# Optimization experiments

Hardware: AMD Instinct MI355X
Metric: run time of the kernel (lower is better)

The kernel has to match this reference:

```python
import jax, jax.numpy as jnp
import numpy as np

B, S, H, NH = 4, 2048, 1024, 16
HD = H // NH
EPS = 1e-12


def setup_inputs() -> dict:
    key = jax.random.key(0)
    ks = jax.random.split(key, 12)
    sc = 0.02
    return {
        "query": jax.random.normal(ks[0], (B, S, H), dtype=jnp.float32),
        "attention_mask": jnp.zeros((B, 1, 1, S), dtype=jnp.float32),
        "Wq": jax.random.normal(ks[1], (H, H), dtype=jnp.float32) * sc,
        "bq": jnp.zeros((H,), dtype=jnp.float32),
        "Wk": jax.random.normal(ks[2], (H, H), dtype=jnp.float32) * sc,
        "bk": jnp.zeros((H,), dtype=jnp.float32),
        "Wv": jax.random.normal(ks[3], (H, H), dtype=jnp.float32) * sc,
        "bv": jnp.zeros((H,), dtype=jnp.float32),
        "Wd": jax.random.normal(ks[4], (H, H), dtype=jnp.float32) * sc,
        "bd": jnp.zeros((H,), dtype=jnp.float32),
        "ln_gamma": jnp.ones((H,), dtype=jnp.float32),
        "ln_beta": jnp.zeros((H,), dtype=jnp.float32),
    }


def reference(query, attention_mask, Wq, bq, Wk, bk, Wv, bv, Wd, bd, ln_gamma, ln_beta):
    # QKV projections: [B,S,H] -> [B,S,NH,HD]
    q = (query @ Wq + bq).reshape(B, S, NH, HD)
    k = (query @ Wk + bk).reshape(B, S, NH, HD)
    v = (query @ Wv + bv).reshape(B, S, NH, HD)
    # scores: [B,NH,S,S]
    scores = jnp.einsum("bqhd,bkhd->bhqk", q, k) / jnp.sqrt(jnp.float32(HD))
    scores = scores + attention_mask
    probs = jax.nn.softmax(scores, axis=-1)  # attn_dropout p=0 (eval)
    ctx = jnp.einsum("bhqk,bkhd->bqhd", probs, v).reshape(B, S, H)
    hidden = ctx @ Wd + bd  # out_dropout p=0 (eval)
    # pre-LN residual path: LN(hidden) + query
    mu = jnp.mean(hidden, axis=-1, keepdims=True)
    var = jnp.mean(jnp.square(hidden - mu), axis=-1, keepdims=True)
    hidden = (hidden - mu) * jax.lax.rsqrt(var + EPS) * ln_gamma + ln_beta
    return hidden + query
```

## Files before the change

### kernel.cpp

```cpp
#include <hip/hip_runtime.h>
#include <stdint.h>

#define Bn 4
#define Sn 2048
#define Hn 1024
#define NHn 16
#define Mn 8192

typedef unsigned short bf_t;
typedef __attribute__((ext_vector_type(8))) short s16x8;
typedef __attribute__((ext_vector_type(4))) short s16x4;
typedef __attribute__((ext_vector_type(8))) unsigned short u16x8;
typedef __attribute__((ext_vector_type(4))) unsigned short u16x4;
typedef __attribute__((ext_vector_type(4))) float f32x4;
typedef __attribute__((ext_vector_type(4))) unsigned int u32x4;
typedef __attribute__((ext_vector_type(2))) unsigned int u32x2;

__device__ __forceinline__ bf_t f2bf(float f) {
  unsigned int u = __float_as_uint(f);
  u += 0x7fffu + ((u >> 16) & 1u);
  return (bf_t)(u >> 16);
}

__device__ __forceinline__ unsigned pk2(float lo, float hi) {
  return __builtin_amdgcn_perm(__float_as_uint(hi), __float_as_uint(lo), 0x07060302u);
}
__device__ __forceinline__ s16x4 pack4(float a0, float a1, float a2, float a3) {
  u32x2 t;
  t[0] = pk2(a0, a1);
  t[1] = pk2(a2, a3);
  return __builtin_bit_cast(s16x4, t);
}

#define MFMA16K16(a, b, c) __builtin_amdgcn_mfma_f32_16x16x16bf16_1k(a, b, c, 0, 0, 0)

#define GLOAD16(gp, lp) __builtin_amdgcn_global_load_lds(              \
    (__attribute__((address_space(1))) void*)(gp),                     \
    (__attribute__((address_space(3))) void*)(lp), 16, 0, 0)

__global__ __launch_bounds__(256)
void prep(const float* __restrict__ Wq, const float* __restrict__ Wk,
          const float* __restrict__ Wv, const float* __restrict__ Wd,
          const float* __restrict__ query,
          bf_t* __restrict__ Wt, bf_t* __restrict__ Wdt, bf_t* __restrict__ Xb) {
  __shared__ float tile[32][33];
  const int z = blockIdx.z;
  const int tx = threadIdx.x;
  const int ty = threadIdx.y;
  if (z == 4) {
    const int bid = blockIdx.y * 32 + blockIdx.x;
    const int t = ty * 32 + tx;
    const size_t base = (size_t)bid * 8192 + t * 4;
#pragma unroll
    for (int i = 0; i < 8; i++) {
      const f32x4 v = *(const f32x4*)(query + base + i * 1024);
      u16x4 o;
      o[0] = f2bf(v[0]); o[1] = f2bf(v[1]); o[2] = f2bf(v[2]); o[3] = f2bf(v[3]);
      *(u16x4*)(Xb + base + i * 1024) = o;
    }
    return;
  }
  const float* W = (z == 0) ? Wq : (z == 1) ? Wk : (z == 2) ? Wv : Wd;
  bf_t* dst = (z < 3) ? Wt + (size_t)z * Hn * Hn : Wdt;
  const int n0 = blockIdx.x * 32, k0 = blockIdx.y * 32;
#pragma unroll
  for (int i = 0; i < 4; i++)
    tile[ty + i * 8][tx] = W[(size_t)(k0 + ty + i * 8) * Hn + n0 + tx];
  __syncthreads();
#pragma unroll
  for (int i = 0; i < 4; i++) {
    const int nn = ty + i * 8, kk = tx;
    dst[(size_t)(n0 + nn) * Hn + k0 + kk] = f2bf(tile[kk][nn]);
  }
}

__global__ __launch_bounds__(256, 3)
void gemm_bt(const bf_t* __restrict__ A, const bf_t* __restrict__ Bt,
             const float* __restrict__ b0, const float* __restrict__ b1,
             const float* __restrict__ b2, void* __restrict__ outp,
             int N, int K, int out_bf16)
{
  __shared__ bf_t As[2][4096];
  __shared__ bf_t Bs[2][4096];
  const int tid = threadIdx.x;
  const int wave = tid >> 6, lane = tid & 63;
  const int l15 = lane & 15, quad = lane >> 4;
  const int bm = blockIdx.y * 128, bn = blockIdx.x * 128;
  const int wm = (wave >> 1) * 64, wn = (wave & 1) * 64;
  const int srow = tid >> 2;
  const int scol = (tid & 3) * 8;

  const bf_t* Ag = A + (size_t)(bm + srow) * K + scol;
  const bf_t* Bg = Bt + (size_t)(bn + srow) * K + scol;

  f32x4 acc[4][4] = {};

  GLOAD16(Ag, As[0] + tid * 8);
  GLOAD16(Ag + (size_t)64 * K, As[0] + 2048 + tid * 8);
  GLOAD16(Bg, Bs[0] + tid * 8);
  GLOAD16(Bg + (size_t)64 * K, Bs[0] + 2048 + tid * 8);

  const int nIter = K >> 5;
  for (int i = 0; i < nIter; i++) {
    const int cur = i & 1;
    __syncthreads();
    if (i + 1 < nIter) {
      const int k0 = (i + 1) * 32;
      GLOAD16(Ag + k0, As[cur ^ 1] + tid * 8);
      GLOAD16(Ag + (size_t)64 * K + k0, As[cur ^ 1] + 2048 + tid * 8);
      GLOAD16(Bg + k0, Bs[cur ^ 1] + tid * 8);
      GLOAD16(Bg + (size_t)64 * K + k0, Bs[cur ^ 1] + 2048 + tid * 8);
    }
    s16x8 af[4], bfr[4];
#pragma unroll
    for (int mi = 0; mi < 4; mi++)
      af[mi] = *(const s16x8*)&As[cur][(wm + mi * 16 + l15) * 32 + quad * 8];
#pragma unroll
    for (int ni = 0; ni < 4; ni++)
      bfr[ni] = *(const s16x8*)&Bs[cur][(wn + ni * 16 + l15) * 32 + quad * 8];
#pragma unroll
    for (int mi = 0; mi < 4; mi++)
#pragma unroll
      for (int ni = 0; ni < 4; ni++)
        acc[mi][ni] = __builtin_amdgcn_mfma_f32_16x16x32_bf16(af[mi], bfr[ni], acc[mi][ni], 0, 0, 0);
  }

#pragma unroll
  for (int ni = 0; ni < 4; ni++) {
    const int gn = bn + wn + ni * 16 + l15;
    const float* bp = (gn < 1024) ? b0 : ((gn < 2048) ? b1 : b2);
    const float bias = bp[gn & 1023];
#pragma unroll
    for (int mi = 0; mi < 4; mi++) {
#pragma unroll
      for (int r = 0; r < 4; r++) {
        const int gm = bm + wm + mi * 16 + quad * 4 + r;
        const float v = acc[mi][ni][r] + bias;
        if (out_bf16) ((bf_t*)outp)[(size_t)gm * N + gn] = f2bf(v);
        else          ((float*)outp)[(size_t)gm * N + gn] = v;
      }
    }
  }
}

__global__ __launch_bounds__(256)
void kvswz(const bf_t* __restrict__ qkv, bf_t* __restrict__ Kf,
           bf_t* __restrict__ Vf, const float* __restrict__ mask,
           float* __restrict__ mask2) {
  __shared__ u32x4 smbuf[640];
  const int t = threadIdx.x;
  const int bh = blockIdx.y, b = bh >> 4, h = bh & 15;
  const int k0 = blockIdx.x * 64;

  if (blockIdx.z == 0) {
    bf_t* KT = (bf_t*)smbuf;
#pragma unroll
    for (int i = 0; i < 2; i++) {
      const int c = t + i * 256;
      const int row = c >> 3, col8 = (c & 7) * 8;
      const u16x8 v = *(const u16x8*)(qkv + (size_t)(b * Sn + k0 + row) * 3072 + 1024 + h * 64 + col8);
      *(u16x8*)&KT[row * 80 + col8] = v;
    }
    __syncthreads();
    bf_t* dst0 = Kf + ((size_t)(bh * 32 + blockIdx.x) * 8) * 512;
#pragma unroll
    for (int i = 0; i < 2; i++) {
      const int p = t + i * 256;
      const int frag = p >> 6, lane = p & 63;
      const int ks = frag >> 1, half = frag & 1;
      const int l15 = lane & 15, quad = lane >> 4;
      const u16x8 v = *(const u16x8*)&KT[(ks * 16 + l15) * 80 + half * 32 + quad * 8];
      *(u16x8*)(dst0 + (size_t)frag * 512 + lane * 8) = v;
    }
  } else {
    unsigned int* P32 = (unsigned int*)smbuf;
    {
      const int kp = t >> 3;
      const int d0 = (t & 7) * 8;
      const bf_t* p0 = qkv + (size_t)(b * Sn + k0 + 2 * kp) * 3072 + 2048 + h * 64 + d0;
      const u16x8 r0 = *(const u16x8*)p0;
      const u16x8 r1 = *(const u16x8*)(p0 + 3072);
#pragma unroll
      for (int j = 0; j < 8; j++)
        P32[(d0 + j) * 33 + kp] = (unsigned)r0[j] | ((unsigned)r1[j] << 16);
    }
    if (h == 0 && t < 64)
      mask2[b * Sn + k0 + t] = mask[b * Sn + k0 + t] * 1.44269504f;
    __syncthreads();
    bf_t* dst0 = Vf + ((size_t)(bh * 32 + blockIdx.x) * 8) * 512;
#pragma unroll
    for (int i = 0; i < 2; i++) {
      const int p = t + i * 256;
      const int fp = p >> 6, lane = p & 63;
      const int dvblk = fp >> 1, kpair = fp & 1;
      const int l15 = lane & 15, quad = (lane >> 4) & 3;
      const int d = dvblk * 16 + l15;
      const int c = kpair * 16 + quad * 2;
      u32x4 w;
      w[0] = P32[d * 33 + c];
      w[1] = P32[d * 33 + c + 1];
      w[2] = P32[d * 33 + c + 8];
      w[3] = P32[d * 33 + c + 9];
      *(u32x4*)(dst0 + (size_t)fp * 512 + lane * 8) = w;
    }
  }
}

__global__ __launch_bounds__(256)
void attn(const bf_t* __restrict__ qkv, const bf_t* __restrict__ Kf,
          const bf_t* __restrict__ Vf, const float* __restrict__ mask2,
          bf_t* __restrict__ ctx)
{
  __shared__ bf_t Ks[2][4096];
  __shared__ bf_t Vs[2][4096];
  __shared__ float Ms[2048];

  const int tid = threadIdx.x;
  const int wave = tid >> 6, lane = tid & 63;
  const int l15 = lane & 15, quad = lane >> 4;
  const int idx = blockIdx.x;
  const int bh = idx & 63, b = bh >> 4, h = bh & 15;
  const int q0 = (idx >> 6) * 128;

  {
    const float* m2row = mask2 + (size_t)b * Sn;
    const f32x4 m0 = *(const f32x4*)(m2row + tid * 8);
    const f32x4 m1 = *(const f32x4*)(m2row + tid * 8 + 4);
    *(f32x4*)&Ms[tid * 8] = m0;
    *(f32x4*)&Ms[tid * 8 + 4] = m1;
  }

  s16x8 aq[2][2];
#pragma unroll
  for (int qf = 0; qf < 2; qf++) {
    const bf_t* qp = qkv + (size_t)(b * Sn + q0 + wave * 32 + qf * 16 + l15) * 3072 + h * 64;
    aq[qf][0] = *(const s16x8*)(qp + quad * 8);
    aq[qf][1] = *(const s16x8*)(qp + 32 + quad * 8);
  }

  f32x4 lacc[2] = {};
  f32x4 o[2][4] = {};
  const s16x4 ONES = {16256, 16256, 16256, 16256};

  const bf_t* kb = Kf + (size_t)bh * 32 * 4096;
  const bf_t* vb = Vf + (size_t)bh * 32 * 4096;

  const float C1 = 0.125f * 1.44269504f;

#pragma unroll
  for (int c = 0; c < 2; c++) {
    GLOAD16(kb + c * 2048 + tid * 8, Ks[0] + c * 2048 + tid * 8);
    GLOAD16(vb + c * 2048 + tid * 8, Vs[0] + c * 2048 + tid * 8);
  }

  for (int it = 0; it < 32; ++it) {
    const int cur = it & 1;
    __syncthreads();
    if (it < 31) {
      const bf_t* kn = kb + (size_t)(it + 1) * 4096;
      const bf_t* vn = vb + (size_t)(it + 1) * 4096;
#pragma unroll
      for (int c = 0; c < 2; c++) {
        GLOAD16(kn + c * 2048 + tid * 8, Ks[cur ^ 1] + c * 2048 + tid * 8);
        GLOAD16(vn + c * 2048 + tid * 8, Vs[cur ^ 1] + c * 2048 + tid * 8);
      }
    }

    s16x4 pb[2][4];
#pragma unroll
    for (int e = 0; e < 4; e++) {
      const s16x8 k0f = *(const s16x8*)&Ks[cur][(e * 2 + 0) * 512 + lane * 8];
      const s16x8 k1f = *(const s16x8*)&Ks[cur][(e * 2 + 1) * 512 + lane * 8];
      const f32x4 mk2 = *(const f32x4*)&Ms[it * 64 + e * 16 + quad * 4];
#pragma unroll
      for (int qf = 0; qf < 2; qf++) {
        f32x4 acc = {};
        acc = __builtin_amdgcn_mfma_f32_16x16x32_bf16(k0f, aq[qf][0], acc, 0, 0, 0);
        acc = __builtin_amdgcn_mfma_f32_16x16x32_bf16(k1f, aq[qf][1], acc, 0, 0, 0);
        const float p0 = __builtin_amdgcn_exp2f(fmaf(acc[0], C1, mk2[0]));
        const float p1 = __builtin_amdgcn_exp2f(fmaf(acc[1], C1, mk2[1]));
        const float p2 = __builtin_amdgcn_exp2f(fmaf(acc[2], C1, mk2[2]));
        const float p3 = __builtin_amdgcn_exp2f(fmaf(acc[3], C1, mk2[3]));
        pb[qf][e] = pack4(p0, p1, p2, p3);
        lacc[qf] = MFMA16K16(ONES, pb[qf][e], lacc[qf]);
      }
    }

#pragma unroll
    for (int kpair = 0; kpair < 2; kpair++)
#pragma unroll
      for (int dvblk = 0; dvblk < 4; dvblk++) {
        const s16x8 vv = *(const s16x8*)&Vs[cur][(dvblk * 2 + kpair) * 512 + lane * 8];
        const s16x4 vlo = {vv[0], vv[1], vv[2], vv[3]};
        const s16x4 vhi = {vv[4], vv[5], vv[6], vv[7]};
#pragma unroll
        for (int qf = 0; qf < 2; qf++) {
          o[qf][dvblk] = MFMA16K16(vlo, pb[qf][kpair * 2 + 0], o[qf][dvblk]);
          o[qf][dvblk] = MFMA16K16(vhi, pb[qf][kpair * 2 + 1], o[qf][dvblk]);
        }
      }
  }

#pragma unroll
  for (int qf = 0; qf < 2; qf++) {
    const float inv = 1.f / lacc[qf][0];
    const size_t row = (size_t)(b * Sn + q0 + wave * 32 + qf * 16 + l15);
#pragma unroll
    for (int dvblk = 0; dvblk < 4; dvblk++) {
      u16x4 ov;
#pragma unroll
      for (int r = 0; r < 4; r++) ov[r] = f2bf(o[qf][dvblk][r] * inv);
      *(u16x4*)&ctx[row * Hn + h * 64 + dvblk * 16 + quad * 4] = ov;
    }
  }
}

__global__ __launch_bounds__(256)
void ln_res(const float* __restrict__ hid, const float* __restrict__ query,
            const float* __restrict__ gamma, const float* __restrict__ beta,
            float* __restrict__ out)
{
  const int row = blockIdx.x, t = threadIdx.x;
  const f32x4 h = *(const f32x4*)(hid + (size_t)row * Hn + t * 4);
  float s = h[0] + h[1] + h[2] + h[3];
  float ss = h[0]*h[0] + h[1]*h[1] + h[2]*h[2] + h[3]*h[3];
#pragma unroll
  for (int m = 32; m; m >>= 1) { s += __shfl_xor(s, m); ss += __shfl_xor(ss, m); }
  __shared__ float red[8];
  if ((t & 63) == 0) { red[t >> 6] = s; red[4 + (t >> 6)] = ss; }
  __syncthreads();
  s = red[0] + red[1] + red[2] + red[3];
  ss = red[4] + red[5] + red[6] + red[7];
  const float mu = s * (1.f / Hn);
  const float rs = rsqrtf(ss * (1.f / Hn) - mu * mu + 1e-12f);
  const f32x4 q = *(const f32x4*)(query + (size_t)row * Hn + t * 4);
  const f32x4 g = *(const f32x4*)(gamma + t * 4);
  const f32x4 be = *(const f32x4*)(beta + t * 4);
  f32x4 o;
#pragma unroll
  for (int j = 0; j < 4; j++) o[j] = (h[j] - mu) * rs * g[j] + be[j] + q[j];
  *(f32x4*)(out + (size_t)row * Hn + t * 4) = o;
}

extern "C" void kernel_launch(void* const* d_in, const int* in_sizes, int n_in,
                              void* d_out, int out_size, void* d_ws, size_t ws_size,
                              hipStream_t stream) {
  const float* query = (const float*)d_in[0];
  const float* mask  = (const float*)d_in[1];
  const float* Wq = (const float*)d_in[2];
  const float* bq = (const float*)d_in[3];
  const float* Wk = (const float*)d_in[4];
  const float* bk = (const float*)d_in[5];
  const float* Wv = (const float*)d_in[6];
  const float* bv = (const float*)d_in[7];
  const float* Wd = (const float*)d_in[8];
  const float* bd = (const float*)d_in[9];
  const float* gamma = (const float*)d_in[10];
  const float* beta  = (const float*)d_in[11];

  char* w = (char*)d_ws;
  bf_t* Xb  = (bf_t*)w;  w += (size_t)Mn * Hn * 2;
  bf_t* Wt  = (bf_t*)w;  w += (size_t)3 * Hn * Hn * 2;
  bf_t* Wdt = (bf_t*)w;  w += (size_t)Hn * Hn * 2;
  bf_t* QKV = (bf_t*)w;  w += (size_t)Mn * 3 * Hn * 2;
  bf_t* Vf  = (bf_t*)w;  w += (size_t)64 * 32 * 4096 * 2;
  bf_t* Ctx = (bf_t*)w;  w += (size_t)Mn * Hn * 2;
  bf_t* Kf  = (bf_t*)w;
  float* Hid = (float*)w;  w += (size_t)Mn * Hn * 4;
  float* Mask2 = (float*)w;

  prep<<<dim3(32, 32, 5), dim3(32, 8), 0, stream>>>(Wq, Wk, Wv, Wd, query, Wt, Wdt, Xb);
  gemm_bt<<<dim3(24, 64), 256, 0, stream>>>(Xb, Wt, bq, bk, bv, QKV, 3072, 1024, 1);
  kvswz<<<dim3(32, 64, 2), 256, 0, stream>>>(QKV, Kf, Vf, mask, Mask2);
  attn<<<1024, 256, 0, stream>>>(QKV, Kf, Vf, Mask2, Ctx);
  gemm_bt<<<dim3(8, 64), 256, 0, stream>>>(Ctx, Wdt, bd, bd, bd, Hid, 1024, 1024, 0);
  ln_res<<<Mn, 256, 0, stream>>>(Hid, query, gamma, beta, (float*)d_out);
}
```

Measured before the change: 337.7 us.

## Split attention keys across two wave groups and fold mask into V

The attention kernel now uses 512 threads, with two groups of four waves each processing half of the key sequence. The partial outputs and row sums are merged through shared memory at the end. The mask is pre-exponentiated and folded into V (and into the row-sum MFMA operand), which removes the per-element mask add from the inner loop. The V fragment layout is reordered for the half-tile, and s_setprio hints are added around the MFMA blocks. The goal is more waves to hide latency and less ALU work in the loop. The cost is an extra reduction step, and the mask is now applied multiplicatively in bf16, which adds rounding error.

```diff
diff --git a/kernel.cpp b/kernel.cpp
--- a/kernel.cpp
+++ b/kernel.cpp
@@ -146,7 +146,7 @@
 __global__ __launch_bounds__(256)
 void kvswz(const bf_t* __restrict__ qkv, bf_t* __restrict__ Kf,
            bf_t* __restrict__ Vf, const float* __restrict__ mask,
-           float* __restrict__ mask2) {
+           bf_t* __restrict__ Fb) {
   __shared__ u32x4 smbuf[640];
   const int t = threadIdx.x;
   const int bh = blockIdx.y, b = bh >> 4, h = bh & 15;
@@ -177,15 +177,23 @@
     {
       const int kp = t >> 3;
       const int d0 = (t & 7) * 8;
-      const bf_t* p0 = qkv + (size_t)(b * Sn + k0 + 2 * kp) * 3072 + 2048 + h * 64 + d0;
+      const int kg = k0 + 2 * kp;
+      const float f0 = __builtin_amdgcn_exp2f(mask[b * Sn + kg] * 1.44269504f);
+      const float f1 = __builtin_amdgcn_exp2f(mask[b * Sn + kg + 1] * 1.44269504f);
+      const bf_t* p0 = qkv + (size_t)(b * Sn + kg) * 3072 + 2048 + h * 64 + d0;
       const u16x8 r0 = *(const u16x8*)p0;
       const u16x8 r1 = *(const u16x8*)(p0 + 3072);
 #pragma unroll
-      for (int j = 0; j < 8; j++)
-        P32[(d0 + j) * 33 + kp] = (unsigned)r0[j] | ((unsigned)r1[j] << 16);
-    }
-    if (h == 0 && t < 64)
-      mask2[b * Sn + k0 + t] = mask[b * Sn + k0 + t] * 1.44269504f;
+      for (int j = 0; j < 8; j++) {
+        const float v0 = __uint_as_float((unsigned)r0[j] << 16) * f0;
+        const float v1 = __uint_as_float((unsigned)r1[j] << 16) * f1;
+        P32[(d0 + j) * 33 + kp] = pk2(v0, v1);
+      }
+    }
+    if (h == 0 && t < 64) {
+      const float fm = __builtin_amdgcn_exp2f(mask[b * Sn + k0 + t] * 1.44269504f);
+      Fb[b * Sn + k0 + t] = f2bf(fm);
+    }
     __syncthreads();
     bf_t* dst0 = Vf + ((size_t)(bh * 32 + blockIdx.x) * 8) * 512;
 #pragma unroll
@@ -201,116 +209,124 @@
       w[1] = P32[d * 33 + c + 1];
       w[2] = P32[d * 33 + c + 8];
       w[3] = P32[d * 33 + c + 9];
-      *(u32x4*)(dst0 + (size_t)fp * 512 + lane * 8) = w;
-    }
-  }
-}
-
-__global__ __launch_bounds__(256)
+      *(u32x4*)(dst0 + (size_t)(kpair * 4 + dvblk) * 512 + lane * 8) = w;
+    }
+  }
+}
+
+__global__ __launch_bounds__(512, 8)
 void attn(const bf_t* __restrict__ qkv, const bf_t* __restrict__ Kf,
-          const bf_t* __restrict__ Vf, const float* __restrict__ mask2,
+          const bf_t* __restrict__ Vf, const bf_t* __restrict__ Fb,
           bf_t* __restrict__ ctx)
 {
-  __shared__ bf_t Ks[2][4096];
-  __shared__ bf_t Vs[2][4096];
-  __shared__ float Ms[2048];
+  __shared__ __align__(16) bf_t KV[2][2][2][2048];
+  __shared__ __align__(16) bf_t Fs[2048];
 
   const int tid = threadIdx.x;
   const int wave = tid >> 6, lane = tid & 63;
+  const int g = wave >> 2, wv = wave & 3;
+  const int tg = tid & 255;
   const int l15 = lane & 15, quad = lane >> 4;
   const int idx = blockIdx.x;
   const int bh = idx & 63, b = bh >> 4, h = bh & 15;
   const int q0 = (idx >> 6) * 128;
 
-  {
-    const float* m2row = mask2 + (size_t)b * Sn;
-    const f32x4 m0 = *(const f32x4*)(m2row + tid * 8);
-    const f32x4 m1 = *(const f32x4*)(m2row + tid * 8 + 4);
-    *(f32x4*)&Ms[tid * 8] = m0;
-    *(f32x4*)&Ms[tid * 8 + 4] = m1;
-  }
+  if (tid < 256) GLOAD16(Fb + (size_t)b * Sn + tid * 8, Fs + tid * 8);
 
   s16x8 aq[2][2];
 #pragma unroll
   for (int qf = 0; qf < 2; qf++) {
-    const bf_t* qp = qkv + (size_t)(b * Sn + q0 + wave * 32 + qf * 16 + l15) * 3072 + h * 64;
+    const bf_t* qp = qkv + (size_t)(b * Sn + q0 + wv * 32 + qf * 16 + l15) * 3072 + h * 64;
     aq[qf][0] = *(const s16x8*)(qp + quad * 8);
     aq[qf][1] = *(const s16x8*)(qp + 32 + quad * 8);
   }
 
   f32x4 lacc[2] = {};
   f32x4 o[2][4] = {};
-  const s16x4 ONES = {16256, 16256, 16256, 16256};
-
-  const bf_t* kb = Kf + (size_t)bh * 32 * 4096;
-  const bf_t* vb = Vf + (size_t)bh * 32 * 4096;
-
+
+  const bf_t* kb = Kf + (size_t)bh * 131072 + (size_t)g * 65536;
+  const bf_t* vb = Vf + (size_t)bh * 131072 + (size_t)g * 65536;
   const float C1 = 0.125f * 1.44269504f;
 
-#pragma unroll
-  for (int c = 0; c < 2; c++) {
-    GLOAD16(kb + c * 2048 + tid * 8, Ks[0] + c * 2048 + tid * 8);
-    GLOAD16(vb + c * 2048 + tid * 8, Vs[0] + c * 2048 + tid * 8);
-  }
+  GLOAD16(kb + tg * 8, KV[g][0][0] + tg * 8);
+  GLOAD16(vb + tg * 8, KV[g][1][0] + tg * 8);
 
   for (int it = 0; it < 32; ++it) {
     const int cur = it & 1;
     __syncthreads();
     if (it < 31) {
-      const bf_t* kn = kb + (size_t)(it + 1) * 4096;
-      const bf_t* vn = vb + (size_t)(it + 1) * 4096;
-#pragma unroll
-      for (int c = 0; c < 2; c++) {
-        GLOAD16(kn + c * 2048 + tid * 8, Ks[cur ^ 1] + c * 2048 + tid * 8);
-        GLOAD16(vn + c * 2048 + tid * 8, Vs[cur ^ 1] + c * 2048 + tid * 8);
-      }
-    }
-
-    s16x4 pb[2][4];
-#pragma unroll
-    for (int e = 0; e < 4; e++) {
-      const s16x8 k0f = *(const s16x8*)&Ks[cur][(e * 2 + 0) * 512 + lane * 8];
-      const s16x8 k1f = *(const s16x8*)&Ks[cur][(e * 2 + 1) * 512 + lane * 8];
-      const f32x4 mk2 = *(const f32x4*)&Ms[it * 64 + e * 16 + quad * 4];
+      GLOAD16(kb + (it + 1) * 2048 + tg * 8, KV[g][0][cur ^ 1] + tg * 8);
+      GLOAD16(vb + (it + 1) * 2048 + tg * 8, KV[g][1][cur ^ 1] + tg * 8);
+    }
+
+    s16x4 pb[2][2];
+#pragma unroll
+    for (int e = 0; e < 2; e++) {
+      const s16x8 k0f = *(const s16x8*)&KV[g][0][cur][(e * 2 + 0) * 512 + lane * 8];
+      const s16x8 k1f = *(const s16x8*)&KV[g][0][cur][(e * 2 + 1) * 512 + lane * 8];
+      const s16x4 ff = *(const s16x4*)&Fs[g * 1024 + it * 32 + e * 16 + quad * 4];
 #pragma unroll
       for (int qf = 0; qf < 2; qf++) {
         f32x4 acc = {};
+        __builtin_amdgcn_s_setprio(1);
         acc = __builtin_amdgcn_mfma_f32_16x16x32_bf16(k0f, aq[qf][0], acc, 0, 0, 0);
         acc = __builtin_amdgcn_mfma_f32_16x16x32_bf16(k1f, aq[qf][1], acc, 0, 0, 0);
-        const float p0 = __builtin_amdgcn_exp2f(fmaf(acc[0], C1, mk2[0]));
-        const float p1 = __builtin_amdgcn_exp2f(fmaf(acc[1], C1, mk2[1]));
-        const float p2 = __builtin_amdgcn_exp2f(fmaf(acc[2], C1, mk2[2]));
-        const float p3 = __builtin_amdgcn_exp2f(fmaf(acc[3], C1, mk2[3]));
+        __builtin_amdgcn_s_setprio(0);
+        const float p0 = __builtin_amdgcn_exp2f(acc[0] * C1);
+        const float p1 = __builtin_amdgcn_exp2f(acc[1] * C1);
+        const float p2 = __builtin_amdgcn_exp2f(acc[2] * C1);
+        const float p3 = __builtin_amdgcn_exp2f(acc[3] * C1);
         pb[qf][e] = pack4(p0, p1, p2, p3);
-        lacc[qf] = MFMA16K16(ONES, pb[qf][e], lacc[qf]);
-      }
-    }
-
-#pragma unroll
-    for (int kpair = 0; kpair < 2; kpair++)
+        lacc[qf] = MFMA16K16(ff, pb[qf][e], lacc[qf]);
+      }
+    }
+
+    __builtin_amdgcn_s_setprio(1);
+#pragma unroll
+    for (int dvblk = 0; dvblk < 4; dvblk++) {
+      const s16x8 vv = *(const s16x8*)&KV[g][1][cur][dvblk * 512 + lane * 8];
+      const s16x4 vlo = {vv[0], vv[1], vv[2], vv[3]};
+      const s16x4 vhi = {vv[4], vv[5], vv[6], vv[7]};
+#pragma unroll
+      for (int qf = 0; qf < 2; qf++) {
+        o[qf][dvblk] = MFMA16K16(vlo, pb[qf][0], o[qf][dvblk]);
+        o[qf][dvblk] = MFMA16K16(vhi, pb[qf][1], o[qf][dvblk]);
+      }
+    }
+    __builtin_amdgcn_s_setprio(0);
+  }
+
+  __syncthreads();
+  float* sm = (float*)&KV[0][0][0][0];
+  float* sl = (float*)&Fs[0];
+  if (g == 1) {
+#pragma unroll
+    for (int qf = 0; qf < 2; qf++) {
+      const int row = wv * 32 + qf * 16 + l15;
 #pragma unroll
       for (int dvblk = 0; dvblk < 4; dvblk++) {
-        const s16x8 vv = *(const s16x8*)&Vs[cur][(dvblk * 2 + kpair) * 512 + lane * 8];
-        const s16x4 vlo = {vv[0], vv[1], vv[2], vv[3]};
-        const s16x4 vhi = {vv[4], vv[5], vv[6], vv[7]};
-#pragma unroll
-        for (int qf = 0; qf < 2; qf++) {
-          o[qf][dvblk] = MFMA16K16(vlo, pb[qf][kpair * 2 + 0], o[qf][dvblk]);
-          o[qf][dvblk] = MFMA16K16(vhi, pb[qf][kpair * 2 + 1], o[qf][dvblk]);
-        }
-      }
-  }
-
-#pragma unroll
-  for (int qf = 0; qf < 2; qf++) {
-    const float inv = 1.f / lacc[qf][0];
-    const size_t row = (size_t)(b * Sn + q0 + wave * 32 + qf * 16 + l15);
-#pragma unroll
-    for (int dvblk = 0; dvblk < 4; dvblk++) {
-      u16x4 ov;
-#pragma unroll
-      for (int r = 0; r < 4; r++) ov[r] = f2bf(o[qf][dvblk][r] * inv);
-      *(u16x4*)&ctx[row * Hn + h * 64 + dvblk * 16 + quad * 4] = ov;
+        const int col = (dvblk * 16 + quad * 4 + l15 * 4) & 63;
+        *(f32x4*)&sm[row * 64 + col] = o[qf][dvblk];
+      }
+      if (quad == 0) sl[row] = lacc[qf][0];
+    }
+  }
+  __syncthreads();
+  if (g == 0) {
+#pragma unroll
+    for (int qf = 0; qf < 2; qf++) {
+      const int row = wv * 32 + qf * 16 + l15;
+      const float inv = 1.f / (lacc[qf][0] + sl[row]);
+      const size_t grow = (size_t)(b * Sn + q0 + row);
+#pragma unroll
+      for (int dvblk = 0; dvblk < 4; dvblk++) {
+        const int col = (dvblk * 16 + quad * 4 + l15 * 4) & 63;
+        const f32x4 o2 = *(const f32x4*)&sm[row * 64 + col];
+        u16x4 ov;
+#pragma unroll
+        for (int r = 0; r < 4; r++) ov[r] = f2bf((o[qf][dvblk][r] + o2[r]) * inv);
+        *(u16x4*)&ctx[grow * Hn + h * 64 + dvblk * 16 + quad * 4] = ov;
+      }
     }
   }
 }
@@ -367,12 +383,12 @@
   bf_t* Ctx = (bf_t*)w;  w += (size_t)Mn * Hn * 2;
   bf_t* Kf  = (bf_t*)w;
   float* Hid = (float*)w;  w += (size_t)Mn * Hn * 4;
-  float* Mask2 = (float*)w;
+  bf_t* Fb = (bf_t*)w;
 
   prep<<<dim3(32, 32, 5), dim3(32, 8), 0, stream>>>(Wq, Wk, Wv, Wd, query, Wt, Wdt, Xb);
   gemm_bt<<<dim3(24, 64), 256, 0, stream>>>(Xb, Wt, bq, bk, bv, QKV, 3072, 1024, 1);
-  kvswz<<<dim3(32, 64, 2), 256, 0, stream>>>(QKV, Kf, Vf, mask, Mask2);
-  attn<<<1024, 256, 0, stream>>>(QKV, Kf, Vf, Mask2, Ctx);
+  kvswz<<<dim3(32, 64, 2), 256, 0, stream>>>(QKV, Kf, Vf, mask, Fb);
+  attn<<<1024, 512, 0, stream>>>(QKV, Kf, Vf, Fb, Ctx);
   gemm_bt<<<dim3(8, 64), 256, 0, stream>>>(Ctx, Wdt, bd, bd, bd, Hid, 1024, 1024, 0);
   ln_res<<<Mn, 256, 0, stream>>>(Hid, query, gamma, beta, (float*)d_out);
 }
```

After: 843.4 us. 150% more time.
